# Performance work log

Measured on AMD Instinct MI355X. Metric: run time of the kernel, lower is better.

Reference implementation:

```python
import jax, jax.numpy as jnp
import numpy as np

N_GENES = 2000
D_MODEL = 256
N_LAYERS = 4
D_STATE = 16
D_CONV = 4
EXPAND = 2
D_INNER = EXPAND * D_MODEL  # 512
DT_RANK = (D_MODEL + 15) // 16  # 16


def layer_norm(x, w, b, eps=1e-5):
    mu = jnp.mean(x, axis=-1, keepdims=True)
    var = jnp.mean((x - mu) ** 2, axis=-1, keepdims=True)
    return (x - mu) * jax.lax.rsqrt(var + eps) * w + b


def mamba_mixer(h, in_w, cw, cb, xp_w, dtp_w, dtp_b, A_log, Dvec, out_w):
    # h: [B, L, d_model]
    B, L, _ = h.shape
    xz = jnp.einsum('bld,ed->ble', h, in_w)            # [B,L,2*Di]
    u, z = jnp.split(xz, 2, axis=-1)                    # [B,L,Di] each
    # causal depthwise conv1d (kernel D_CONV)
    up = jnp.pad(u, ((0, 0), (D_CONV - 1, 0), (0, 0)))
    u = sum(up[:, k:k + L, :] * cw[:, k] for k in range(D_CONV)) + cb
    u = jax.nn.silu(u)
    # input-dependent dt, B, C
    xdbc = jnp.einsum('bld,ed->ble', u, xp_w)           # [B,L,dt_rank+2N]
    dt_r = xdbc[..., :DT_RANK]
    Bm = xdbc[..., DT_RANK:DT_RANK + D_STATE]           # [B,L,N]
    Cm = xdbc[..., DT_RANK + D_STATE:]                  # [B,L,N]
    dt = jax.nn.softplus(jnp.einsum('blr,dr->bld', dt_r, dtp_w) + dtp_b)  # [B,L,Di]
    A = -jnp.exp(A_log)                                 # [Di,N]
    dA = jnp.exp(dt[..., None] * A)                     # [B,L,Di,N]
    dBu = dt[..., None] * Bm[:, :, None, :] * u[..., None]

    def step(hst, inp):
        a, bu = inp
        hst = a * hst + bu
        return hst, hst

    h0 = jnp.zeros((B, D_INNER, D_STATE), dA.dtype)
    _, hs = jax.lax.scan(step, h0, (jnp.moveaxis(dA, 1, 0), jnp.moveaxis(dBu, 1, 0)))
    y = jnp.einsum('lbdn,lbn->bld', hs, jnp.moveaxis(Cm, 1, 0)) + u * Dvec
    y = y * jax.nn.silu(z)
    return jnp.einsum('bld,ed->ble', y, out_w)          # [B,L,d_model]


def setup_inputs() -> dict:
    key = jax.random.key(0)
    ks = jax.random.split(key, 16)
    nl = N_LAYERS
    inp = {
        'x': jax.random.normal(ks[0], (2, N_GENES), jnp.float32),
        'bulk_in_w': jax.random.normal(ks[1], (D_MODEL,), jnp.float32),
        'bulk_in_b': jnp.zeros((D_MODEL,), jnp.float32),
        'gene_emb': jax.random.normal(ks[2], (1, N_GENES, D_MODEL), jnp.float32) * 0.02,
        'mod_emb': jax.random.normal(ks[3], (1, 1, D_MODEL), jnp.float32) * 0.02,
        'ln_w': jnp.ones((nl, D_MODEL), jnp.float32),
        'ln_b': jnp.zeros((nl, D_MODEL), jnp.float32),
        'in_proj_w': jax.random.normal(ks[4], (nl, 2 * D_INNER, D_MODEL), jnp.float32) * (D_MODEL ** -0.5),
        'conv_w': jax.random.normal(ks[5], (nl, D_INNER, D_CONV), jnp.float32) * (D_CONV ** -0.5),
        'conv_b': jnp.zeros((nl, D_INNER), jnp.float32),
        'x_proj_w': jax.random.normal(ks[6], (nl, DT_RANK + 2 * D_STATE, D_INNER), jnp.float32) * (D_INNER ** -0.5),
        'dt_proj_w': jax.random.normal(ks[7], (nl, D_INNER, DT_RANK), jnp.float32) * 0.01,
        'dt_proj_b': jnp.full((nl, D_INNER), -4.0, jnp.float32),
        'A_log': jnp.broadcast_to(jnp.log(jnp.arange(1, D_STATE + 1, dtype=jnp.float32)), (nl, D_INNER, D_STATE)).copy(),
        'D': jnp.ones((nl, D_INNER), jnp.float32),
        'out_proj_w': jax.random.normal(ks[8], (nl, D_MODEL, D_INNER), jnp.float32) * (D_INNER ** -0.5),
        'fin_w': jnp.ones((D_MODEL,), jnp.float32),
        'fin_b': jnp.zeros((D_MODEL,), jnp.float32),
        'head_w': jax.random.normal(ks[9], (D_MODEL,), jnp.float32) * (D_MODEL ** -0.5),
        'head_b': jnp.zeros((), jnp.float32),
    }
    return inp


def reference(x, bulk_in_w, bulk_in_b, gene_emb, mod_emb, ln_w, ln_b, in_proj_w,
              conv_w, conv_b, x_proj_w, dt_proj_w, dt_proj_b, A_log, D, out_proj_w,
              fin_w, fin_b, head_w, head_b):
    # token embed (modality='bulk'); Linear(1,d_model) == x[...,None]*w + b
    h = x[..., None] * bulk_in_w + bulk_in_b + gene_emb + mod_emb  # [B,L,d_model]
    for i in range(N_LAYERS):
        h = h + mamba_mixer(layer_norm(h, ln_w[i], ln_b[i]), in_proj_w[i], conv_w[i],
                            conv_b[i], x_proj_w[i], dt_proj_w[i], dt_proj_b[i],
                            A_log[i], D[i], out_proj_w[i])
    h = layer_norm(h, fin_w, fin_b)
    y = jnp.einsum('bld,d->bl', h, head_w) + head_b  # bulk head, squeeze(-1)
    return y
```

## Files before the change

### kernel.cpp

```cpp
#include <hip/hip_runtime.h>
#include <math.h>

#define B_  2
#define L_  2000
#define DM_ 256
#define DI_ 512
#define DS_ 16
#define NL_ 4
#define BL_ (B_*L_)
#define BLP_ 4096
#define NC_ 125
#define CL_ 16
#define NST_ (B_*DI_*DS_)

typedef unsigned short ushort_t;
typedef __attribute__((ext_vector_type(8))) short bf16x8;
typedef __attribute__((ext_vector_type(4))) float f32x4;

__device__ __forceinline__ float siluf(float x) {
    return x / (1.f + __expf(-x));
}

__device__ __forceinline__ ushort_t f2bf(float x) {
    unsigned int u = __float_as_uint(x);
    unsigned int r = (u + 0x7FFFu + ((u >> 16) & 1u)) >> 16;
    return (ushort_t)r;
}

__device__ __forceinline__ float bf2f(ushort_t v) {
    return __uint_as_float(((unsigned int)v) << 16);
}

__global__ __launch_bounds__(256) void embed_f2bf_kernel(
    const float* __restrict__ x, const float* __restrict__ biw,
    const float* __restrict__ bib, const float* __restrict__ ge,
    const float* __restrict__ me, float* __restrict__ h,
    float2* __restrict__ stats,
    const float* __restrict__ s0, const float* __restrict__ s1,
    const float* __restrict__ s2, ushort_t* __restrict__ d0,
    ushort_t* __restrict__ d1, ushort_t* __restrict__ d2,
    int N0, int N1, int N2)
{
    if (blockIdx.x < BL_) {
        __shared__ float sm[8];
        int bl = blockIdx.x, d = threadIdx.x;
        int l = bl % L_;
        float v = x[bl]*biw[d] + bib[d] + ge[(size_t)l*DM_ + d] + me[d];
        h[(size_t)bl*DM_ + d] = v;
        float s = v, q = v*v;
        #pragma unroll
        for (int o = 32; o > 0; o >>= 1) {
            s += __shfl_down(s, o);
            q += __shfl_down(q, o);
        }
        if ((d & 63) == 0) { sm[d >> 6] = s; sm[4 + (d >> 6)] = q; }
        __syncthreads();
        if (d == 0) {
            stats[bl] = make_float2(sm[0]+sm[1]+sm[2]+sm[3], sm[4]+sm[5]+sm[6]+sm[7]);
            stats[BLP_ + bl]   = make_float2(0.f, 0.f);
            stats[2*BLP_ + bl] = make_float2(0.f, 0.f);
            stats[3*BLP_ + bl] = make_float2(0.f, 0.f);
        }
    } else {
        int i = (blockIdx.x - BL_)*256 + threadIdx.x;
        const float* s; ushort_t* d; int j;
        if (i < N0)           { s = s0; d = d0; j = i; }
        else if (i < N0+N1)   { s = s1; d = d1; j = i - N0; }
        else if (i < N0+N1+N2){ s = s2; d = d2; j = i - N0 - N1; }
        else return;
        float4 v = *(const float4*)(s + 4*j);
        ushort_t o[4] = {f2bf(v.x), f2bf(v.y), f2bf(v.z), f2bf(v.w)};
        *(ushort2*)(d + 4*j)     = *(ushort2*)&o[0];
        *(ushort2*)(d + 4*j + 2) = *(ushort2*)&o[2];
    }
}

__global__ __launch_bounds__(256) void gemm_ln_mfma(
    const float* __restrict__ H, const float2* __restrict__ stats,
    const float* __restrict__ lnw, const float* __restrict__ lnb,
    const ushort_t* __restrict__ W, ushort_t* __restrict__ C, int ldc)
{
    __shared__ ushort_t a_s[128*64];
    __shared__ ushort_t b_s[128*64];
    const int r0 = blockIdx.x*128, c0 = blockIdx.y*128;
    const int tid = threadIdx.x;
    const int lane = tid & 63, w = tid >> 6;
    const int wm = (w & 1)*64, wn = (w >> 1)*64;
    const int qd = lane >> 4, l16 = lane & 15;
    f32x4 acc[4][4] = {};
    for (int kc = 0; kc < DM_; kc += 64) {
        #pragma unroll
        for (int q = 0; q < 4; q++) {
            int ch = tid + 256*q;
            int row = ch >> 3, col8 = (ch & 7)*8;
            int grow = r0 + row;
            float2 t0 = stats[grow], t1 = stats[BLP_ + grow];
            float2 t2 = stats[2*BLP_ + grow], t3 = stats[3*BLP_ + grow];
            float sum = t0.x + t1.x + t2.x + t3.x;
            float ssq = t0.y + t1.y + t2.y + t3.y;
            float mu  = sum * (1.f/DM_);
            float inv = rsqrtf(fmaxf(ssq*(1.f/DM_) - mu*mu, 0.f) + 1e-5f);
            const float* hp = H + (size_t)grow*DM_ + kc + col8;
            float4 h0 = *(const float4*)hp, h1 = *(const float4*)(hp + 4);
            const float* wp = lnw + kc + col8;
            const float* bp = lnb + kc + col8;
            float4 w0 = *(const float4*)wp, w1 = *(const float4*)(wp + 4);
            float4 b0 = *(const float4*)bp, b1 = *(const float4*)(bp + 4);
            __align__(16) ushort_t o[8];
            o[0] = f2bf((h0.x - mu)*inv*w0.x + b0.x);
            o[1] = f2bf((h0.y - mu)*inv*w0.y + b0.y);
            o[2] = f2bf((h0.z - mu)*inv*w0.z + b0.z);
            o[3] = f2bf((h0.w - mu)*inv*w0.w + b0.w);
            o[4] = f2bf((h1.x - mu)*inv*w1.x + b1.x);
            o[5] = f2bf((h1.y - mu)*inv*w1.y + b1.y);
            o[6] = f2bf((h1.z - mu)*inv*w1.z + b1.z);
            o[7] = f2bf((h1.w - mu)*inv*w1.w + b1.w);
            *(uint4*)&a_s[row*64 + col8] = *(const uint4*)o;
            *(bf16x8*)&b_s[row*64 + col8] =
                *(const bf16x8*)(W + (size_t)(c0 + row)*DM_ + kc + col8);
        }
        __syncthreads();
        #pragma unroll
        for (int ks = 0; ks < 2; ks++) {
            bf16x8 af[4], bf[4];
            #pragma unroll
            for (int i = 0; i < 4; i++)
                af[i] = *(const bf16x8*)&a_s[(wm + i*16 + l16)*64 + ks*32 + qd*8];
            #pragma unroll
            for (int j = 0; j < 4; j++)
                bf[j] = *(const bf16x8*)&b_s[(wn + j*16 + l16)*64 + ks*32 + qd*8];
            #pragma unroll
            for (int i = 0; i < 4; i++) {
                #pragma unroll
                for (int j = 0; j < 4; j++)
                    acc[i][j] = __builtin_amdgcn_mfma_f32_16x16x32_bf16(
                        af[i], bf[j], acc[i][j], 0, 0, 0);
            }
        }
        __syncthreads();
    }
    #pragma unroll
    for (int i = 0; i < 4; i++) {
        #pragma unroll
        for (int j = 0; j < 4; j++) {
            #pragma unroll
            for (int r = 0; r < 4; r++) {
                int row = r0 + wm + i*16 + qd*4 + r;
                int col = c0 + wn + j*16 + l16;
                C[(size_t)row*ldc + col] = f2bf(acc[i][j][r]);
            }
        }
    }
}

__global__ __launch_bounds__(256) void conv_xproj_kernel(
    const ushort_t* __restrict__ xz, const float* __restrict__ cw,
    const float* __restrict__ cb, const ushort_t* __restrict__ XWb,
    const float* __restrict__ DTW, const float* __restrict__ DTB,
    const float* __restrict__ Alog,
    ushort_t* __restrict__ u_bf, float* __restrict__ bn,
    float* __restrict__ cn, ushort_t* __restrict__ dtn,
    float2* __restrict__ sa)
{
    __shared__ ushort_t xs[19][520];
    __shared__ ushort_t us[16][520];
    __shared__ float ps[4*16*48];
    __shared__ float dtr_s[16][16];
    const int c = blockIdx.x, b = blockIdx.y;
    const int l0 = c * 16;
    const int tid = threadIdx.x;
    const int lane = tid & 63, w = tid >> 6;
    const int qd = lane >> 4, l16 = lane & 15;
    for (int f = tid; f < 19*64; f += 256) {
        int row = f >> 6, c8 = (f & 63)*8;
        int l = l0 - 3 + row;
        uint4 v = {0u, 0u, 0u, 0u};
        if (l >= 0)
            v = *(const uint4*)(xz + (size_t)(b*L_ + l)*1024 + c8);
        *(uint4*)&xs[row][c8] = v;
    }
    __syncthreads();
    #pragma unroll
    for (int q = 0; q < 2; q++) {
        int ch = tid + q*256;
        float4 wv = *(const float4*)(cw + ch*4);
        float bias = cb[ch];
        float x0 = bf2f(xs[0][ch]);
        float x1 = bf2f(xs[1][ch]);
        float x2 = bf2f(xs[2][ch]);
        #pragma unroll
        for (int j = 0; j < 16; j++) {
            float x3 = bf2f(xs[3 + j][ch]);
            float v = fmaf(x0, wv.x, fmaf(x1, wv.y, fmaf(x2, wv.z, fmaf(x3, wv.w, bias))));
            us[j][ch] = f2bf(siluf(v));
            x0 = x1; x1 = x2; x2 = x3;
        }
    }
    __syncthreads();
    for (int f = tid; f < 16*64; f += 256) {
        int row = f >> 6, c8 = (f & 63)*8;
        *(uint4*)(u_bf + (size_t)(b*L_ + l0 + row)*512 + c8) =
            *(const uint4*)&us[row][c8];
    }
    f32x4 acc[3] = {};
    #pragma unroll
    for (int step = 0; step < 4; step++) {
        int k = w*128 + step*32 + qd*8;
        bf16x8 af = *(const bf16x8*)&us[l16][k];
        #pragma unroll
        for (int j = 0; j < 3; j++) {
            bf16x8 bf = *(const bf16x8*)(XWb + (size_t)(j*16 + l16)*512 + k);
            acc[j] = __builtin_amdgcn_mfma_f32_16x16x32_bf16(af, bf, acc[j], 0, 0, 0);
        }
    }
    #pragma unroll
    for (int j = 0; j < 3; j++) {
        #pragma unroll
        for (int r = 0; r < 4; r++)
            ps[(w*16 + qd*4 + r)*48 + j*16 + l16] = acc[j][r];
    }
    __syncthreads();
    #pragma unroll
    for (int e = tid; e < 768; e += 256)
        ps[e] = ps[e] + ps[768 + e] + ps[1536 + e] + ps[2304 + e];
    __syncthreads();
    {
        int row = tid >> 4, n = tid & 15;
        dtr_s[row][n] = ps[row*48 + n];
        size_t base = ((size_t)(b*L_) + l0 + row)*DS_ + n;
        bn[base] = ps[row*48 + 16 + n];
        cn[base] = ps[row*48 + 32 + n];
    }
    __syncthreads();
    #pragma unroll
    for (int q = 0; q < 2; q++) {
        int d = tid + q*256;
        float wreg[16];
        const float4* wp = (const float4*)(DTW + (size_t)d*16);
        #pragma unroll
        for (int k4 = 0; k4 < 4; k4++) {
            float4 v = wp[k4];
            wreg[4*k4+0] = v.x; wreg[4*k4+1] = v.y;
            wreg[4*k4+2] = v.z; wreg[4*k4+3] = v.w;
        }
        float bias = DTB[d];
        float dtv[16];
        #pragma unroll
        for (int r = 0; r < 16; r++) {
            float a = bias;
            #pragma unroll
            for (int k = 0; k < 16; k++) a = fmaf(dtr_s[r][k], wreg[k], a);
            float dt = a > 20.f ? a : log1pf(__expf(a));
            ushort_t dtb16 = f2bf(dt);
            dtn[((size_t)(b*L_) + l0 + r)*DI_ + d] = dtb16;
            dtv[r] = bf2f(dtb16);
        }
        float Ac[DS_], s[DS_], ap[DS_];
        const float* ar = Alog + (size_t)d*DS_;
        #pragma unroll
        for (int n = 0; n < DS_; n++) { Ac[n] = -__expf(ar[n]); s[n] = 0.f; ap[n] = 1.f; }
        #pragma unroll
        for (int l = 0; l < 16; l++) {
            float dt = dtv[l];
            float u  = bf2f(us[l][d]);
            float dtu = dt*u;
            #pragma unroll
            for (int n = 0; n < DS_; n++) {
                float e = __expf(dt*Ac[n]);
                s[n] = fmaf(e, s[n], dtu*ps[l*48 + 16 + n]);
                ap[n] *= e;
            }
        }
        size_t ib = (((size_t)c*B_ + b)*DI_ + d)*DS_;
        float2* sap = sa + ib;
        #pragma unroll
        for (int k = 0; k < 8; k++) {
            float4 t = make_float4(s[2*k], ap[2*k], s[2*k+1], ap[2*k+1]);
            *(float4*)&sap[2*k] = t;
        }
    }
}

__global__ __launch_bounds__(64) void scan_phase2(
    const float2* __restrict__ sa, float* __restrict__ sinc)
{
    const int t = blockIdx.x*64 + threadIdx.x;
    float s = 0.f;
    for (int g = 0; g < 5; g++) {
        float2 v[25];
        #pragma unroll
        for (int i = 0; i < 25; i++)
            v[i] = sa[(size_t)(g*25 + i)*NST_ + t];
        #pragma unroll
        for (int i = 0; i < 25; i++) {
            sinc[(size_t)(g*25 + i)*NST_ + t] = s;
            s = fmaf(v[i].y, s, v[i].x);
        }
    }
}

template<int LAST>
__global__ __launch_bounds__(512) void phase3_fused(
    const ushort_t* __restrict__ dtn, const ushort_t* __restrict__ u_bf,
    const float* __restrict__ bn, const float* __restrict__ cn,
    const float* __restrict__ Alog, const float* __restrict__ Dv,
    const float* __restrict__ sinc, const ushort_t* __restrict__ xz,
    const ushort_t* __restrict__ opw, float* __restrict__ h,
    const float* __restrict__ lnw, const float* __restrict__ lnb,
    const ushort_t* __restrict__ ipw, ushort_t* __restrict__ xz_out,
    const float* __restrict__ hw, const float* __restrict__ hb,
    float* __restrict__ out)
{
    __shared__ float b_sh[CL_*DS_];
    __shared__ float c_sh[CL_*DS_];
    __shared__ ushort_t ys[16][520];
    __shared__ ushort_t a_sh[16][264];
    __shared__ float2 red2[8*16];
    __shared__ float2 muv[16];
    const int c = blockIdx.x, b = blockIdx.y;
    const int l0 = c*CL_;
    const int tid = threadIdx.x;
    const int w = tid >> 6, lane = tid & 63;
    const int qd = lane >> 4, l16 = lane & 15;
    {
        int f = tid & 255;
        size_t src = ((size_t)(b*L_) + l0)*DS_ + f;
        if (tid < 256) b_sh[f] = bn[src];
        else           c_sh[f] = cn[src];
    }
    const int d = tid;
    float Ac[DS_], s[DS_];
    {
        const float* ar = Alog + (size_t)d*DS_;
        #pragma unroll
        for (int n = 0; n < DS_; n++) Ac[n] = -__expf(ar[n]);
        size_t base = (((size_t)c*B_ + b)*DI_ + d)*DS_;
        #pragma unroll
        for (int n4 = 0; n4 < 4; n4++)
            *(float4*)&s[4*n4] = *(const float4*)(sinc + base + 4*n4);
    }
    const float Dd = Dv[d];
    __syncthreads();
    const ushort_t* dtp = dtn  + ((size_t)(b*L_ + l0))*DI_ + d;
    const ushort_t* up  = u_bf + ((size_t)(b*L_ + l0))*DI_ + d;
    const ushort_t* zp  = xz   + ((size_t)(b*L_ + l0))*1024 + 512 + d;
    for (int l = 0; l < CL_; l++) {
        float dt = bf2f(dtp[(size_t)l*DI_]);
        float u  = bf2f(up[(size_t)l*DI_]);
        float z  = bf2f(zp[(size_t)l*1024]);
        float dtu = dt*u;
        float y = u*Dd;
        #pragma unroll
        for (int n = 0; n < DS_; n++) {
            float e = __expf(dt*Ac[n]);
            s[n] = fmaf(e, s[n], dtu*b_sh[l*DS_ + n]);
            y = fmaf(s[n], c_sh[l*DS_ + n], y);
        }
        ys[l][d] = f2bf(y * siluf(z));
    }
    __syncthreads();
    f32x4 acc[2] = {};
    #pragma unroll
    for (int ks = 0; ks < 16; ks++) {
        bf16x8 af = *(const bf16x8*)&ys[l16][ks*32 + qd*8];
        #pragma unroll
        for (int j = 0; j < 2; j++) {
            bf16x8 bfv = *(const bf16x8*)(opw + (size_t)(w*32 + j*16 + l16)*DI_ + ks*32 + qd*8);
            acc[j] = __builtin_amdgcn_mfma_f32_16x16x32_bf16(af, bfv, acc[j], 0, 0, 0);
        }
    }
    float v[2][4];
    #pragma unroll
    for (int r = 0; r < 4; r++) {
        int lrow = qd*4 + r;
        size_t gr = (size_t)(b*L_ + l0 + lrow);
        float sm = 0.f, sq = 0.f;
        #pragma unroll
        for (int j = 0; j < 2; j++) {
            int col = w*32 + j*16 + l16;
            size_t idx = gr*DM_ + col;
            float vv = h[idx] + acc[j][r];
            if (!LAST) h[idx] = vv;
            v[j][r] = vv;
            sm += vv; sq += vv*vv;
        }
        sm += __shfl_xor(sm, 1); sq += __shfl_xor(sq, 1);
        sm += __shfl_xor(sm, 2); sq += __shfl_xor(sq, 2);
        sm += __shfl_xor(sm, 4); sq += __shfl_xor(sq, 4);
        sm += __shfl_xor(sm, 8); sq += __shfl_xor(sq, 8);
        if (l16 == 0) red2[w*16 + lrow] = make_float2(sm, sq);
    }
    __syncthreads();
    if (tid < 16) {
        float sm = 0.f, sq = 0.f;
        #pragma unroll
        for (int ww = 0; ww < 8; ww++) {
            float2 t = red2[ww*16 + tid];
            sm += t.x; sq += t.y;
        }
        float mu  = sm*(1.f/DM_);
        float inv = rsqrtf(fmaxf(sq*(1.f/DM_) - mu*mu, 0.f) + 1e-5f);
        muv[tid] = make_float2(mu, inv);
    }
    __syncthreads();
    if (!LAST) {
        #pragma unroll
        for (int r = 0; r < 4; r++) {
            int lrow = qd*4 + r;
            float2 mi = muv[lrow];
            #pragma unroll
            for (int j = 0; j < 2; j++) {
                int col = w*32 + j*16 + l16;
                a_sh[lrow][col] = f2bf((v[j][r] - mi.x)*mi.y*lnw[col] + lnb[col]);
            }
        }
        __syncthreads();
        f32x4 acc2[8] = {};
        const int n0 = w*128;
        #pragma unroll
        for (int ks = 0; ks < 8; ks++) {
            bf16x8 af = *(const bf16x8*)&a_sh[l16][ks*32 + qd*8];
            #pragma unroll
            for (int j2 = 0; j2 < 8; j2++) {
                bf16x8 bfv = *(const bf16x8*)(ipw + (size_t)(n0 + j2*16 + l16)*DM_ + ks*32 + qd*8);
                acc2[j2] = __builtin_amdgcn_mfma_f32_16x16x32_bf16(af, bfv, acc2[j2], 0, 0, 0);
            }
        }
        #pragma unroll
        for (int j2 = 0; j2 < 8; j2++) {
            #pragma unroll
            for (int r = 0; r < 4; r++) {
                size_t row = (size_t)(b*L_ + l0 + qd*4 + r);
                xz_out[row*1024 + n0 + j2*16 + l16] = f2bf(acc2[j2][r]);
            }
        }
    } else {
        float hd[4];
        #pragma unroll
        for (int r = 0; r < 4; r++) {
            int lrow = qd*4 + r;
            float2 mi = muv[lrow];
            float a = 0.f;
            #pragma unroll
            for (int j = 0; j < 2; j++) {
                int col = w*32 + j*16 + l16;
                float nv = (v[j][r] - mi.x)*mi.y*lnw[col] + lnb[col];
                a = fmaf(nv, hw[col], a);
            }
            hd[r] = a;
        }
        #pragma unroll
        for (int r = 0; r < 4; r++) {
            float x = hd[r];
            x += __shfl_xor(x, 1); x += __shfl_xor(x, 2);
            x += __shfl_xor(x, 4); x += __shfl_xor(x, 8);
            if (l16 == 0) red2[w*16 + qd*4 + r].x = x;
        }
        __syncthreads();
        if (tid < 16) {
            float x = 0.f;
            #pragma unroll
            for (int ww = 0; ww < 8; ww++) x += red2[ww*16 + tid].x;
            out[(size_t)(b*L_) + l0 + tid] = x + hb[0];
        }
    }
}

extern "C" void kernel_launch(void* const* d_in, const int* in_sizes, int n_in,
                              void* d_out, int out_size, void* d_ws, size_t ws_size,
                              hipStream_t stream)
{
    const float* x    = (const float*)d_in[0];
    const float* biw  = (const float*)d_in[1];
    const float* bib  = (const float*)d_in[2];
    const float* ge   = (const float*)d_in[3];
    const float* me   = (const float*)d_in[4];
    const float* lnw  = (const float*)d_in[5];
    const float* lnb  = (const float*)d_in[6];
    const float* ipw  = (const float*)d_in[7];
    const float* cw   = (const float*)d_in[8];
    const float* cb   = (const float*)d_in[9];
    const float* xpw  = (const float*)d_in[10];
    const float* dtw  = (const float*)d_in[11];
    const float* dtb  = (const float*)d_in[12];
    const float* alog = (const float*)d_in[13];
    const float* Dv   = (const float*)d_in[14];
    const float* opw  = (const float*)d_in[15];
    const float* fw   = (const float*)d_in[16];
    const float* fb   = (const float*)d_in[17];
    const float* hw   = (const float*)d_in[18];
    const float* hb   = (const float*)d_in[19];
    float* out = (float*)d_out;

    float* ws  = (float*)d_ws;
    float* h      = ws;
    float2* stats = (float2*)(h + (size_t)BLP_*DM_);
    float* bn     = (float*)(stats + 4*BLP_);
    float* cn     = bn + (size_t)B_*L_*DS_;
    float2* sa    = (float2*)(cn + (size_t)B_*L_*DS_);
    float* sinc   = (float*)(sa + (size_t)NC_*NST_);
    ushort_t* xz_bf = (ushort_t*)(sinc + (size_t)NC_*NST_);
    ushort_t* u_bf  = xz_bf + (size_t)BLP_*1024;
    ushort_t* dtn   = u_bf + (size_t)BLP_*DI_;
    ushort_t* ipwb  = dtn + (size_t)B_*L_*DI_;
    ushort_t* opwb  = ipwb + (size_t)NL_*1024*DM_;
    ushort_t* xpwb  = opwb + (size_t)NL_*DM_*DI_;

    const int N0 = NL_*1024*DM_/4, N1 = NL_*DM_*DI_/4, N2 = NL_*48*512/4;
    const int conv_blocks = (N0+N1+N2 + 255)/256;
    embed_f2bf_kernel<<<BL_ + conv_blocks, 256, 0, stream>>>(
        x, biw, bib, ge, me, h, stats,
        ipw, opw, xpw, ipwb, opwb, xpwb, N0, N1, N2);

    gemm_ln_mfma<<<dim3(BLP_/128, 1024/128), 256, 0, stream>>>(
        h, stats, lnw, lnb, ipwb, xz_bf, 1024);

    for (int i = 0; i < NL_; i++) {
        conv_xproj_kernel<<<dim3(NC_, B_), 256, 0, stream>>>(
            xz_bf, cw + i*DI_*4, cb + i*DI_, xpwb + (size_t)i*48*512,
            dtw + (size_t)i*DI_*16, dtb + i*DI_, alog + (size_t)i*DI_*DS_,
            u_bf, bn, cn, dtn, sa);
        scan_phase2<<<NST_/64, 64, 0, stream>>>(sa, sinc);
        if (i < NL_-1) {
            phase3_fused<0><<<dim3(NC_, B_), 512, 0, stream>>>(
                dtn, u_bf, bn, cn, alog + (size_t)i*DI_*DS_, Dv + i*DI_,
                sinc, xz_bf, opwb + (size_t)i*DM_*DI_, h,
                lnw + (i+1)*DM_, lnb + (i+1)*DM_,
                ipwb + (size_t)(i+1)*1024*DM_, xz_bf,
                nullptr, nullptr, nullptr);
        } else {
            phase3_fused<1><<<dim3(NC_, B_), 512, 0, stream>>>(
                dtn, u_bf, bn, cn, alog + (size_t)i*DI_*DS_, Dv + i*DI_,
                sinc, xz_bf, opwb + (size_t)i*DM_*DI_, h,
                fw, fb,
                nullptr, xz_bf,
                hw, hb, out);
        }
    }
}
```

Before: 414.3 us.

## Widen conv/xproj to 512 threads and stage phase3 inputs in shared memory

The conv+x_proj kernel now runs with 512 threads, one channel per thread, and splits the x_proj K reduction across 8 waves with an 8-way shared-memory partial sum. Phase3 now loads dt, u and z tiles into shared memory with coalesced 16-byte loads instead of strided per-thread global reads in the scan loop, and keeps per-step y values in registers. Unions reuse LDS between phases to limit the footprint. The unused partial LN stats slots are also removed. Risks include higher register pressure from y_reg and the wider block, plus extra barriers.

```diff
diff --git a/kernel.cpp b/kernel.cpp
--- a/kernel.cpp
+++ b/kernel.cpp
@@ -9,24 +9,19 @@
 #define NL_ 4
 #define BL_ (B_*L_)
 #define BLP_ 4096
-#define NC_ 125
-#define CL_ 16
+#define NC_  125
+#define CL_  16
 #define NST_ (B_*DI_*DS_)
 
 typedef unsigned short ushort_t;
 typedef __attribute__((ext_vector_type(8))) short bf16x8;
 typedef __attribute__((ext_vector_type(4))) float f32x4;
 
-__device__ __forceinline__ float siluf(float x) {
-    return x / (1.f + __expf(-x));
-}
-
+__device__ __forceinline__ float siluf(float x) { return x / (1.f + __expf(-x)); }
 __device__ __forceinline__ ushort_t f2bf(float x) {
     unsigned int u = __float_as_uint(x);
-    unsigned int r = (u + 0x7FFFu + ((u >> 16) & 1u)) >> 16;
-    return (ushort_t)r;
-}
-
+    return (ushort_t)((u + 0x7FFFu + ((u >> 16) & 1u)) >> 16);
+}
 __device__ __forceinline__ float bf2f(ushort_t v) {
     return __uint_as_float(((unsigned int)v) << 16);
 }
@@ -55,12 +50,8 @@
         }
         if ((d & 63) == 0) { sm[d >> 6] = s; sm[4 + (d >> 6)] = q; }
         __syncthreads();
-        if (d == 0) {
+        if (d == 0)
             stats[bl] = make_float2(sm[0]+sm[1]+sm[2]+sm[3], sm[4]+sm[5]+sm[6]+sm[7]);
-            stats[BLP_ + bl]   = make_float2(0.f, 0.f);
-            stats[2*BLP_ + bl] = make_float2(0.f, 0.f);
-            stats[3*BLP_ + bl] = make_float2(0.f, 0.f);
-        }
     } else {
         int i = (blockIdx.x - BL_)*256 + threadIdx.x;
         const float* s; ushort_t* d; int j;
@@ -78,7 +69,7 @@
 __global__ __launch_bounds__(256) void gemm_ln_mfma(
     const float* __restrict__ H, const float2* __restrict__ stats,
     const float* __restrict__ lnw, const float* __restrict__ lnb,
-    const ushort_t* __restrict__ W, ushort_t* __restrict__ C, int ldc)
+    const ushort_t* __restrict__ W, ushort_t* __restrict__ C)
 {
     __shared__ ushort_t a_s[128*64];
     __shared__ ushort_t b_s[128*64];
@@ -94,12 +85,9 @@
             int ch = tid + 256*q;
             int row = ch >> 3, col8 = (ch & 7)*8;
             int grow = r0 + row;
-            float2 t0 = stats[grow], t1 = stats[BLP_ + grow];
-            float2 t2 = stats[2*BLP_ + grow], t3 = stats[3*BLP_ + grow];
-            float sum = t0.x + t1.x + t2.x + t3.x;
-            float ssq = t0.y + t1.y + t2.y + t3.y;
-            float mu  = sum * (1.f/DM_);
-            float inv = rsqrtf(fmaxf(ssq*(1.f/DM_) - mu*mu, 0.f) + 1e-5f);
+            float2 t0 = stats[grow];
+            float mu  = t0.x * (1.f/DM_);
+            float inv = rsqrtf(fmaxf(t0.y*(1.f/DM_) - mu*mu, 0.f) + 1e-5f);
             const float* hp = H + (size_t)grow*DM_ + kc + col8;
             float4 h0 = *(const float4*)hp, h1 = *(const float4*)(hp + 4);
             const float* wp = lnw + kc + col8;
@@ -147,13 +135,13 @@
             for (int r = 0; r < 4; r++) {
                 int row = r0 + wm + i*16 + qd*4 + r;
                 int col = c0 + wn + j*16 + l16;
-                C[(size_t)row*ldc + col] = f2bf(acc[i][j][r]);
-            }
-        }
-    }
-}
-
-__global__ __launch_bounds__(256) void conv_xproj_kernel(
+                C[(size_t)row*1024 + col] = f2bf(acc[i][j][r]);
+            }
+        }
+    }
+}
+
+__global__ __launch_bounds__(512) void conv_xproj512(
     const ushort_t* __restrict__ xz, const float* __restrict__ cw,
     const float* __restrict__ cb, const ushort_t* __restrict__ XWb,
     const float* __restrict__ DTW, const float* __restrict__ DTB,
@@ -164,25 +152,22 @@
 {
     __shared__ ushort_t xs[19][520];
     __shared__ ushort_t us[16][520];
-    __shared__ float ps[4*16*48];
+    __shared__ float ps[8*768];
     __shared__ float dtr_s[16][16];
-    const int c = blockIdx.x, b = blockIdx.y;
-    const int l0 = c * 16;
+    const int c = blockIdx.x, b = blockIdx.y, l0 = c*CL_;
     const int tid = threadIdx.x;
     const int lane = tid & 63, w = tid >> 6;
     const int qd = lane >> 4, l16 = lane & 15;
-    for (int f = tid; f < 19*64; f += 256) {
+    for (int f = tid; f < 19*64; f += 512) {
         int row = f >> 6, c8 = (f & 63)*8;
         int l = l0 - 3 + row;
-        uint4 v = {0u, 0u, 0u, 0u};
-        if (l >= 0)
-            v = *(const uint4*)(xz + (size_t)(b*L_ + l)*1024 + c8);
+        uint4 v = {0u,0u,0u,0u};
+        if (l >= 0) v = *(const uint4*)(xz + (size_t)(b*L_ + l)*1024 + c8);
         *(uint4*)&xs[row][c8] = v;
     }
     __syncthreads();
-    #pragma unroll
-    for (int q = 0; q < 2; q++) {
-        int ch = tid + q*256;
+    {
+        int ch = tid;
         float4 wv = *(const float4*)(cw + ch*4);
         float bias = cb[ch];
         float x0 = bf2f(xs[0][ch]);
@@ -197,34 +182,35 @@
         }
     }
     __syncthreads();
-    for (int f = tid; f < 16*64; f += 256) {
+    for (int f = tid; f < 16*64; f += 512) {
         int row = f >> 6, c8 = (f & 63)*8;
         *(uint4*)(u_bf + (size_t)(b*L_ + l0 + row)*512 + c8) =
             *(const uint4*)&us[row][c8];
     }
     f32x4 acc[3] = {};
     #pragma unroll
-    for (int step = 0; step < 4; step++) {
-        int k = w*128 + step*32 + qd*8;
+    for (int st = 0; st < 2; st++) {
+        int k = w*64 + st*32 + qd*8;
         bf16x8 af = *(const bf16x8*)&us[l16][k];
         #pragma unroll
         for (int j = 0; j < 3; j++) {
-            bf16x8 bf = *(const bf16x8*)(XWb + (size_t)(j*16 + l16)*512 + k);
-            acc[j] = __builtin_amdgcn_mfma_f32_16x16x32_bf16(af, bf, acc[j], 0, 0, 0);
-        }
-    }
-    #pragma unroll
-    for (int j = 0; j < 3; j++) {
+            bf16x8 bv = *(const bf16x8*)(XWb + (size_t)(j*16 + l16)*512 + k);
+            acc[j] = __builtin_amdgcn_mfma_f32_16x16x32_bf16(af, bv, acc[j], 0, 0, 0);
+        }
+    }
+    #pragma unroll
+    for (int j = 0; j < 3; j++)
         #pragma unroll
         for (int r = 0; r < 4; r++)
-            ps[(w*16 + qd*4 + r)*48 + j*16 + l16] = acc[j][r];
-    }
-    __syncthreads();
-    #pragma unroll
-    for (int e = tid; e < 768; e += 256)
-        ps[e] = ps[e] + ps[768 + e] + ps[1536 + e] + ps[2304 + e];
-    __syncthreads();
-    {
+            ps[w*768 + (qd*4 + r)*48 + j*16 + l16] = acc[j][r];
+    __syncthreads();
+    for (int e = tid; e < 768; e += 512) {
+        float v = ps[e] + ps[768+e] + ps[1536+e] + ps[2304+e]
+                + ps[3072+e] + ps[3840+e] + ps[4608+e] + ps[5376+e];
+        ps[e] = v;
+    }
+    __syncthreads();
+    if (tid < 256) {
         int row = tid >> 4, n = tid & 15;
         dtr_s[row][n] = ps[row*48 + n];
         size_t base = ((size_t)(b*L_) + l0 + row)*DS_ + n;
@@ -232,9 +218,8 @@
         cn[base] = ps[row*48 + 32 + n];
     }
     __syncthreads();
-    #pragma unroll
-    for (int q = 0; q < 2; q++) {
-        int d = tid + q*256;
+    {
+        const int d = tid;
         float wreg[16];
         const float4* wp = (const float4*)(DTW + (size_t)d*16);
         #pragma unroll
@@ -274,10 +259,8 @@
         size_t ib = (((size_t)c*B_ + b)*DI_ + d)*DS_;
         float2* sap = sa + ib;
         #pragma unroll
-        for (int k = 0; k < 8; k++) {
-            float4 t = make_float4(s[2*k], ap[2*k], s[2*k+1], ap[2*k+1]);
-            *(float4*)&sap[2*k] = t;
-        }
+        for (int k = 0; k < 8; k++)
+            *(float4*)&sap[2*k] = make_float4(s[2*k], ap[2*k], s[2*k+1], ap[2*k+1]);
     }
 }
 
@@ -314,11 +297,11 @@
     __shared__ float b_sh[CL_*DS_];
     __shared__ float c_sh[CL_*DS_];
     __shared__ ushort_t ys[16][520];
-    __shared__ ushort_t a_sh[16][264];
-    __shared__ float2 red2[8*16];
+    __shared__ union { ushort_t dt_t[16][520]; ushort_t z_t[16][520]; } T0;
+    __shared__ union { ushort_t u_t[16][520];  ushort_t a_sh[16][264]; } T1;
+    __shared__ float2 red2[128];
     __shared__ float2 muv[16];
-    const int c = blockIdx.x, b = blockIdx.y;
-    const int l0 = c*CL_;
+    const int c = blockIdx.x, b = blockIdx.y, l0 = c*CL_;
     const int tid = threadIdx.x;
     const int w = tid >> 6, lane = tid & 63;
     const int qd = lane >> 4, l16 = lane & 15;
@@ -328,6 +311,14 @@
         if (tid < 256) b_sh[f] = bn[src];
         else           c_sh[f] = cn[src];
     }
+    {
+        const int r = tid >> 5, cb16 = (tid & 31)*16;
+        size_t rb = ((size_t)(b*L_) + l0 + r)*DI_ + cb16;
+        *(uint4*)&T0.dt_t[r][cb16]     = *(const uint4*)(dtn + rb);
+        *(uint4*)&T0.dt_t[r][cb16 + 8] = *(const uint4*)(dtn + rb + 8);
+        *(uint4*)&T1.u_t[r][cb16]      = *(const uint4*)(u_bf + rb);
+        *(uint4*)&T1.u_t[r][cb16 + 8]  = *(const uint4*)(u_bf + rb + 8);
+    }
     const int d = tid;
     float Ac[DS_], s[DS_];
     {
@@ -341,13 +332,11 @@
     }
     const float Dd = Dv[d];
     __syncthreads();
-    const ushort_t* dtp = dtn  + ((size_t)(b*L_ + l0))*DI_ + d;
-    const ushort_t* up  = u_bf + ((size_t)(b*L_ + l0))*DI_ + d;
-    const ushort_t* zp  = xz   + ((size_t)(b*L_ + l0))*1024 + 512 + d;
+    float y_reg[CL_];
+    #pragma unroll
     for (int l = 0; l < CL_; l++) {
-        float dt = bf2f(dtp[(size_t)l*DI_]);
-        float u  = bf2f(up[(size_t)l*DI_]);
-        float z  = bf2f(zp[(size_t)l*1024]);
+        float dt = bf2f(T0.dt_t[l][d]);
+        float u  = bf2f(T1.u_t[l][d]);
         float dtu = dt*u;
         float y = u*Dd;
         #pragma unroll
@@ -356,8 +345,19 @@
             s[n] = fmaf(e, s[n], dtu*b_sh[l*DS_ + n]);
             y = fmaf(s[n], c_sh[l*DS_ + n], y);
         }
-        ys[l][d] = f2bf(y * siluf(z));
-    }
+        y_reg[l] = y;
+    }
+    __syncthreads();
+    {
+        const int r = tid >> 5, cb16 = (tid & 31)*16;
+        size_t rb = ((size_t)(b*L_) + l0 + r)*1024 + 512 + cb16;
+        *(uint4*)&T0.z_t[r][cb16]     = *(const uint4*)(xz + rb);
+        *(uint4*)&T0.z_t[r][cb16 + 8] = *(const uint4*)(xz + rb + 8);
+    }
+    __syncthreads();
+    #pragma unroll
+    for (int l = 0; l < CL_; l++)
+        ys[l][d] = f2bf(y_reg[l] * siluf(bf2f(T0.z_t[l][d])));
     __syncthreads();
     f32x4 acc[2] = {};
     #pragma unroll
@@ -365,8 +365,8 @@
         bf16x8 af = *(const bf16x8*)&ys[l16][ks*32 + qd*8];
         #pragma unroll
         for (int j = 0; j < 2; j++) {
-            bf16x8 bfv = *(const bf16x8*)(opw + (size_t)(w*32 + j*16 + l16)*DI_ + ks*32 + qd*8);
-            acc[j] = __builtin_amdgcn_mfma_f32_16x16x32_bf16(af, bfv, acc[j], 0, 0, 0);
+            bf16x8 bv = *(const bf16x8*)(opw + (size_t)(w*32 + j*16 + l16)*DI_ + ks*32 + qd*8);
+            acc[j] = __builtin_amdgcn_mfma_f32_16x16x32_bf16(af, bv, acc[j], 0, 0, 0);
         }
     }
     float v[2][4];
@@ -411,7 +411,7 @@
             #pragma unroll
             for (int j = 0; j < 2; j++) {
                 int col = w*32 + j*16 + l16;
-                a_sh[lrow][col] = f2bf((v[j][r] - mi.x)*mi.y*lnw[col] + lnb[col]);
+                T1.a_sh[lrow][col] = f2bf((v[j][r] - mi.x)*mi.y*lnw[col] + lnb[col]);
             }
         }
         __syncthreads();
@@ -419,11 +419,11 @@
         const int n0 = w*128;
         #pragma unroll
         for (int ks = 0; ks < 8; ks++) {
-            bf16x8 af = *(const bf16x8*)&a_sh[l16][ks*32 + qd*8];
+            bf16x8 af = *(const bf16x8*)&T1.a_sh[l16][ks*32 + qd*8];
             #pragma unroll
             for (int j2 = 0; j2 < 8; j2++) {
-                bf16x8 bfv = *(const bf16x8*)(ipw + (size_t)(n0 + j2*16 + l16)*DM_ + ks*32 + qd*8);
-                acc2[j2] = __builtin_amdgcn_mfma_f32_16x16x32_bf16(af, bfv, acc2[j2], 0, 0, 0);
+                bf16x8 bv = *(const bf16x8*)(ipw + (size_t)(n0 + j2*16 + l16)*DM_ + ks*32 + qd*8);
+                acc2[j2] = __builtin_amdgcn_mfma_f32_16x16x32_bf16(af, bv, acc2[j2], 0, 0, 0);
             }
         }
         #pragma unroll
@@ -440,28 +440,28 @@
         for (int r = 0; r < 4; r++) {
             int lrow = qd*4 + r;
             float2 mi = muv[lrow];
-            float a = 0.f;
+            float aa = 0.f;
             #pragma unroll
             for (int j = 0; j < 2; j++) {
                 int col = w*32 + j*16 + l16;
                 float nv = (v[j][r] - mi.x)*mi.y*lnw[col] + lnb[col];
-                a = fmaf(nv, hw[col], a);
-            }
-            hd[r] = a;
+                aa = fmaf(nv, hw[col], aa);
+            }
+            hd[r] = aa;
         }
         #pragma unroll
         for (int r = 0; r < 4; r++) {
-            float x = hd[r];
-            x += __shfl_xor(x, 1); x += __shfl_xor(x, 2);
-            x += __shfl_xor(x, 4); x += __shfl_xor(x, 8);
-            if (l16 == 0) red2[w*16 + qd*4 + r].x = x;
+            float xv = hd[r];
+            xv += __shfl_xor(xv, 1); xv += __shfl_xor(xv, 2);
+            xv += __shfl_xor(xv, 4); xv += __shfl_xor(xv, 8);
+            if (l16 == 0) red2[w*16 + qd*4 + r].x = xv;
         }
         __syncthreads();
         if (tid < 16) {
-            float x = 0.f;
-            #pragma unroll
-            for (int ww = 0; ww < 8; ww++) x += red2[ww*16 + tid].x;
-            out[(size_t)(b*L_) + l0 + tid] = x + hb[0];
+            float xv = 0.f;
+            #pragma unroll
+            for (int ww = 0; ww < 8; ww++) xv += red2[ww*16 + tid].x;
+            out[(size_t)(b*L_) + l0 + tid] = xv + hb[0];
         }
     }
 }
@@ -495,7 +495,7 @@
     float* ws  = (float*)d_ws;
     float* h      = ws;
     float2* stats = (float2*)(h + (size_t)BLP_*DM_);
-    float* bn     = (float*)(stats + 4*BLP_);
+    float* bn     = (float*)(stats + BLP_);
     float* cn     = bn + (size_t)B_*L_*DS_;
     float2* sa    = (float2*)(cn + (size_t)B_*L_*DS_);
     float* sinc   = (float*)(sa + (size_t)NC_*NST_);
@@ -513,10 +513,10 @@
         ipw, opw, xpw, ipwb, opwb, xpwb, N0, N1, N2);
 
     gemm_ln_mfma<<<dim3(BLP_/128, 1024/128), 256, 0, stream>>>(
-        h, stats, lnw, lnb, ipwb, xz_bf, 1024);
+        h, stats, lnw, lnb, ipwb, xz_bf);
 
     for (int i = 0; i < NL_; i++) {
-        conv_xproj_kernel<<<dim3(NC_, B_), 256, 0, stream>>>(
+        conv_xproj512<<<dim3(NC_, B_), 512, 0, stream>>>(
             xz_bf, cw + i*DI_*4, cb + i*DI_, xpwb + (size_t)i*48*512,
             dtw + (size_t)i*DI_*16, dtb + i*DI_, alog + (size_t)i*DI_*DS_,
             u_bf, bn, cn, dtn, sa);
```

Result: faster. 393.7 us (-5.0%).
